# Optimization experiments

Hardware: AMD Instinct MI355X
Metric: run time of the kernel (lower is better)

Reference implementation:

```python
import jax, jax.numpy as jnp
import numpy as np

B, C, N = 2, 1024, 80
D = 3 * C + 2  # 3074 token dim
DFF = 2048     # torch TransformerEncoderLayer default dim_feedforward
HW = 224
REFINE = 3
EPS = 1e-5


def _layernorm(x, g, b):
    m = jnp.mean(x, axis=-1, keepdims=True)
    v = jnp.mean((x - m) ** 2, axis=-1, keepdims=True)
    return g * (x - m) / jnp.sqrt(v + EPS) + b


def _pos_encoding(seq_len, dim):
    pos = jnp.arange(seq_len, dtype=jnp.float32)[:, None]
    div = jnp.exp(jnp.arange(0, dim, 2, dtype=jnp.float32) * (-np.log(10000.0) / dim))
    pe = jnp.zeros((seq_len, dim), dtype=jnp.float32)
    pe = pe.at[:, 0::2].set(jnp.sin(pos * div)).at[:, 1::2].set(jnp.cos(pos * div))
    return pe


def _forward(pre_f, curr_f, first_f, ln_g, ln_b, ipw, ipb, opw, opb,
             n1g, n1b, l1w, l1b, l2w, l2b, n2g, n2b, ow, ob,
             prev_b, first_b):
    # --- vectorized find_best_shift: batched circular L1 correlation ---
    idx = (jnp.arange(N)[None, :] - jnp.arange(N)[:, None]) % N  # [shift, pos]
    rolled = first_b[:, idx]                                     # [B, N, N, 2]
    dist = jnp.abs(prev_b[:, None] - rolled).sum(axis=(-1, -2))  # [B, N]
    best = jnp.argmin(dist, axis=1)                              # first min, like torch loop
    roll_idx = (jnp.arange(N)[None, :] - best[:, None]) % N      # [B, N]
    first_b = jax.vmap(lambda fb, ri: fb[ri])(first_b, roll_idx)

    # --- bilinear upsample to 224x224 (F.interpolate, align_corners=False) ---
    up = lambda f: jax.image.resize(f, (f.shape[0], f.shape[1], HW, HW), method='bilinear')
    pre_up, curr_up, first_up = up(pre_f), up(curr_f), up(first_f)

    # --- vectorized get_bou_features: [B,N,C] gather ---
    gather = jax.vmap(lambda f, b: f[:, b[:, 0], b[:, 1]].T)
    pre_q = gather(pre_up, prev_b)      # [B, N, C]
    first_q = gather(first_up, first_b)  # [B, N, C]

    pe = _pos_encoding(N, D)
    curr = prev_b.astype(jnp.float32)
    scale = 1.0 / jnp.sqrt(jnp.float32(D))
    results = []
    for _ in range(REFINE):
        bf = gather(curr_up, curr.astype(jnp.int32))          # [B, N, C]
        tokens = jnp.concatenate([pre_q, bf, curr, first_q], axis=-1)  # [B, N, D]
        tokens = _layernorm(tokens, ln_g, ln_b)
        tokens = tokens + pe[None]
        # --- TransformerEncoderLayer (post-norm, nhead=1, relu, eval/no dropout) ---
        qkv = tokens @ ipw.T + ipb
        q, k, v = jnp.split(qkv, 3, axis=-1)
        attn = jax.nn.softmax(jnp.einsum('bqd,bkd->bqk', q, k) * scale, axis=-1)
        a = jnp.einsum('bqk,bkd->bqd', attn, v) @ opw.T + opb
        x = _layernorm(tokens + a, n1g, n1b)
        ff = jax.nn.relu(x @ l1w.T + l1b) @ l2w.T + l2b
        x = _layernorm(x + ff, n2g, n2b)
        out = x @ ow.T + ob                                   # [B, N, 1026]
        curr = jnp.clip(curr + out[..., C:], 0.0, 223.0)
        pre_q = pre_q + out[..., :C]
        results.append(curr)
    return jnp.stack(results)  # [REFINE, B, N, 2]


def setup_inputs() -> dict:
    key = jax.random.key(0)
    ks = jax.random.split(key, 12)
    f = lambda i, s: jax.random.normal(ks[i], s, dtype=jnp.float32)
    w = lambda i, s: 0.02 * jax.random.normal(ks[i], s, dtype=jnp.float32)
    return {
        'pre_img_features': f(0, (B, C, 14, 14)),
        'curr_img_features': f(1, (B, C, 14, 14)),
        'first_img_features': f(2, (B, C, 14, 14)),
        'previous_boundary': jax.random.randint(ks[3], (B, N, 2), 0, HW),
        'first_boundary': jax.random.randint(ks[4], (B, N, 2), 0, HW),
        'ln_g': jnp.ones((D,), jnp.float32), 'ln_b': jnp.zeros((D,), jnp.float32),
        'in_proj_w': w(5, (3 * D, D)), 'in_proj_b': jnp.zeros((3 * D,), jnp.float32),
        'out_proj_w': w(6, (D, D)), 'out_proj_b': jnp.zeros((D,), jnp.float32),
        'norm1_g': jnp.ones((D,), jnp.float32), 'norm1_b': jnp.zeros((D,), jnp.float32),
        'lin1_w': w(7, (DFF, D)), 'lin1_b': jnp.zeros((DFF,), jnp.float32),
        'lin2_w': w(8, (D, DFF)), 'lin2_b': jnp.zeros((D,), jnp.float32),
        'norm2_g': jnp.ones((D,), jnp.float32), 'norm2_b': jnp.zeros((D,), jnp.float32),
        'out_w': w(9, (C + 2, D)), 'out_b': jnp.zeros((C + 2,), jnp.float32),
    }


def reference(pre_img_features, curr_img_features, first_img_features,
              previous_boundary, first_boundary,
              ln_g, ln_b, in_proj_w, in_proj_b, out_proj_w, out_proj_b,
              norm1_g, norm1_b, lin1_w, lin1_b, lin2_w, lin2_b,
              norm2_g, norm2_b, out_w, out_b):
    return _forward(pre_img_features, curr_img_features, first_img_features,
                    ln_g, ln_b, in_proj_w, in_proj_b, out_proj_w, out_proj_b,
                    norm1_g, norm1_b, lin1_w, lin1_b, lin2_w, lin2_b,
                    norm2_g, norm2_b, out_w, out_b,
                    previous_boundary, first_boundary)
```

## Files before the change

### kernel.cpp

```cpp
#include <hip/hip_runtime.h>
#include <math.h>

#define B_    2
#define C_    1024
#define N_    80
#define D_    3074
#define DFF_  2048
#define OD_   1026
#define QKV_  9222
#define M_    160
#define EPS_  1e-5f
#define KPD_  3104

typedef __attribute__((ext_vector_type(8))) short bf16x8;
typedef __attribute__((ext_vector_type(4))) float f32x4;

__device__ inline short f2bf(float f) {
    unsigned u = __float_as_uint(f);
    u += 0x7fffu + ((u >> 16) & 1u);
    return (short)(u >> 16);
}

__device__ inline float wave_sum(float v) {
#pragma unroll
    for (int off = 32; off > 0; off >>= 1) v += __shfl_down(v, off, 64);
    return v;
}

__device__ inline float wave_max(float v) {
#pragma unroll
    for (int off = 32; off > 0; off >>= 1) v = fmaxf(v, __shfl_down(v, off, 64));
    return v;
}

__device__ inline void block_reduce_2(float& s, float& s2, float* red) {
    int tid = threadIdx.x;
    int lane = tid & 63, wid = tid >> 6;
    s = wave_sum(s);
    s2 = wave_sum(s2);
    if (lane == 0) { red[wid] = s; red[4 + wid] = s2; }
    __syncthreads();
    if (tid == 0) {
        red[8] = red[0] + red[1] + red[2] + red[3];
        red[9] = red[4] + red[5] + red[6] + red[7];
    }
    __syncthreads();
    s = red[8]; s2 = red[9];
}

__device__ inline void bilin_setup(int p, int& i0, int& i1, float& t) {
    float s = (p + 0.5f) * 0.0625f - 0.5f;
    s = fminf(fmaxf(s, 0.0f), 13.0f);
    i0 = (int)s;
    t = s - (float)i0;
    i1 = min(i0 + 1, 13);
}

__device__ inline float bilin_tap(const float* f, int y0, int y1, float ty,
                                  int x0, int x1, float tx) {
    float a = f[y0 * 14 + x0], b = f[y0 * 14 + x1];
    float c = f[y1 * 14 + x0], d = f[y1 * 14 + x1];
    return (1.f - ty) * ((1.f - tx) * a + tx * b) + ty * ((1.f - tx) * c + tx * d);
}

__global__ __launch_bounds__(128) void align_kernel(const int* __restrict__ prev_b,
                                                    const int* __restrict__ first_b,
                                                    int* __restrict__ fb_al) {
    int b = blockIdx.x;
    int tid = threadIdx.x;
    __shared__ int dist[N_];
    __shared__ int bestIdx;
    if (tid < N_) {
        int s = 0;
        for (int j = 0; j < N_; ++j) {
            int src = (j - tid) % N_;
            if (src < 0) src += N_;
            int dy = prev_b[(b * N_ + j) * 2] - first_b[(b * N_ + src) * 2];
            int dx = prev_b[(b * N_ + j) * 2 + 1] - first_b[(b * N_ + src) * 2 + 1];
            s += abs(dy) + abs(dx);
        }
        dist[tid] = s;
    }
    __syncthreads();
    if (tid == 0) {
        int best = 0, bd = dist[0];
        for (int i = 1; i < N_; ++i)
            if (dist[i] < bd) { bd = dist[i]; best = i; }
        bestIdx = best;
    }
    __syncthreads();
    if (tid < N_) {
        int src = (tid - bestIdx) % N_;
        if (src < 0) src += N_;
        fb_al[(b * N_ + tid) * 2]     = first_b[(b * N_ + src) * 2];
        fb_al[(b * N_ + tid) * 2 + 1] = first_b[(b * N_ + src) * 2 + 1];
    }
}

__global__ __launch_bounds__(256) void gather_init_kernel(
        const float* __restrict__ pre_f, const float* __restrict__ first_f,
        const int* __restrict__ prev_b, const int* __restrict__ fb_al,
        float* __restrict__ pre_q, float* __restrict__ first_q,
        float* __restrict__ curr) {
    int m = blockIdx.x;
    int b = m / N_;
    int tid = threadIdx.x;
    int py = prev_b[m * 2], px = prev_b[m * 2 + 1];
    int fy = fb_al[m * 2], fx = fb_al[m * 2 + 1];
    int py0, py1, px0, px1, fy0, fy1, fx0, fx1;
    float pty, ptx, fty, ftx;
    bilin_setup(py, py0, py1, pty);
    bilin_setup(px, px0, px1, ptx);
    bilin_setup(fy, fy0, fy1, fty);
    bilin_setup(fx, fx0, fx1, ftx);
    for (int c = tid; c < C_; c += 256) {
        const float* fp = pre_f + (size_t)(b * C_ + c) * 196;
        const float* ff = first_f + (size_t)(b * C_ + c) * 196;
        pre_q[(size_t)m * C_ + c]   = bilin_tap(fp, py0, py1, pty, px0, px1, ptx);
        first_q[(size_t)m * C_ + c] = bilin_tap(ff, fy0, fy1, fty, fx0, fx1, ftx);
    }
    if (tid < 2) curr[m * 2 + tid] = (float)prev_b[m * 2 + tid];
}

__global__ __launch_bounds__(256) void tokens_kernel(
        const float* __restrict__ curr_f, const float* __restrict__ pre_q,
        const float* __restrict__ first_q, const float* __restrict__ curr,
        const float* __restrict__ ln_g, const float* __restrict__ ln_b,
        float* __restrict__ tokens, short* __restrict__ tokens_bf) {
    int m = blockIdx.x;
    int b = m / N_;
    int n = m % N_;
    int tid = threadIdx.x;
    __shared__ float bf[C_];
    __shared__ float red[10];

    float cy = curr[m * 2], cx = curr[m * 2 + 1];
    int iy = (int)cy, ix = (int)cx;
    int y0, y1, x0, x1;
    float ty, tx;
    bilin_setup(iy, y0, y1, ty);
    bilin_setup(ix, x0, x1, tx);
    for (int c = tid; c < C_; c += 256) {
        const float* f = curr_f + (size_t)(b * C_ + c) * 196;
        bf[c] = bilin_tap(f, y0, y1, ty, x0, x1, tx);
    }
    __syncthreads();

    float s = 0.f, s2 = 0.f;
    for (int d = tid; d < D_; d += 256) {
        float v;
        if (d < C_)            v = pre_q[(size_t)m * C_ + d];
        else if (d < 2 * C_)   v = bf[d - C_];
        else if (d == 2 * C_)  v = cy;
        else if (d == 2*C_+1)  v = cx;
        else                   v = first_q[(size_t)m * C_ + (d - 2 * C_ - 2)];
        s += v; s2 += v * v;
    }
    block_reduce_2(s, s2, red);
    float mean = s / (float)D_;
    float var = s2 / (float)D_ - mean * mean;
    float inv = rsqrtf(var + EPS_);

    const float negLogDivD = -logf(10000.0f) / (float)D_;
    for (int d = tid; d < KPD_; d += 256) {
        if (d < D_) {
            float v;
            if (d < C_)            v = pre_q[(size_t)m * C_ + d];
            else if (d < 2 * C_)   v = bf[d - C_];
            else if (d == 2 * C_)  v = cy;
            else if (d == 2*C_+1)  v = cx;
            else                   v = first_q[(size_t)m * C_ + (d - 2 * C_ - 2)];
            float ln = ln_g[d] * (v - mean) * inv + ln_b[d];
            int kk = d >> 1;
            float ang = (float)n * expf((float)(2 * kk) * negLogDivD);
            float pe = (d & 1) ? cosf(ang) : sinf(ang);
            float val = ln + pe;
            tokens[(size_t)m * D_ + d] = val;
            tokens_bf[(size_t)m * KPD_ + d] = f2bf(val);
        } else {
            tokens_bf[(size_t)m * KPD_ + d] = 0;
        }
    }
}

__global__ __launch_bounds__(256) void gemm_mfma_sk(
        const short* __restrict__ A, const float* __restrict__ Wf,
        const float* __restrict__ bias, float* __restrict__ Cout,
        int K, int KpA, int O, int KC) {
    int kc0 = blockIdx.y * KC;
    if (kc0 >= K) return;
    int kend = min(K, kc0 + KC);

    int lane = threadIdx.x & 63;
    int wave = threadIdx.x >> 6;
    int col  = lane & 15;
    int quad = lane >> 4;
    int o0 = blockIdx.x * 128 + wave * 32 + col;
    int o1 = o0 + 16;
    int oc0 = min(o0, O - 1), oc1 = min(o1, O - 1);

    const float* wrow0 = Wf + (size_t)oc0 * K + quad * 8;
    const float* wrow1 = Wf + (size_t)oc1 * K + quad * 8;
    const short* abase = A + (size_t)col * KpA + quad * 8;

    f32x4 acc0[10], acc1[10];
#pragma unroll
    for (int t = 0; t < 10; ++t)
#pragma unroll
        for (int r = 0; r < 4; ++r) { acc0[t][r] = 0.f; acc1[t][r] = 0.f; }

    int nfull = (kend - kc0) >> 5;
    bf16x8 aCur[10];
    float2 wCur[8];
    if (nfull > 0) {
#pragma unroll
        for (int t = 0; t < 10; ++t)
            aCur[t] = *(const bf16x8*)(abase + (size_t)t * 16 * KpA + kc0);
#pragma unroll
        for (int j = 0; j < 4; ++j) {
            wCur[j]     = *(const float2*)(wrow0 + kc0 + 2 * j);
            wCur[4 + j] = *(const float2*)(wrow1 + kc0 + 2 * j);
        }
    }
    for (int i = 0; i < nfull; ++i) {
        bf16x8 aNxt[10];
        float2 wNxt[8];
        if (i + 1 < nfull) {
            int kn = kc0 + (i + 1) * 32;
#pragma unroll
            for (int t = 0; t < 10; ++t)
                aNxt[t] = *(const bf16x8*)(abase + (size_t)t * 16 * KpA + kn);
#pragma unroll
            for (int j = 0; j < 4; ++j) {
                wNxt[j]     = *(const float2*)(wrow0 + kn + 2 * j);
                wNxt[4 + j] = *(const float2*)(wrow1 + kn + 2 * j);
            }
        }
        bf16x8 b0, b1;
#pragma unroll
        for (int j = 0; j < 4; ++j) {
            b0[2*j] = f2bf(wCur[j].x);     b0[2*j+1] = f2bf(wCur[j].y);
            b1[2*j] = f2bf(wCur[4+j].x);   b1[2*j+1] = f2bf(wCur[4+j].y);
        }
#pragma unroll
        for (int t = 0; t < 10; ++t) {
            acc0[t] = __builtin_amdgcn_mfma_f32_16x16x32_bf16(aCur[t], b0, acc0[t], 0, 0, 0);
            acc1[t] = __builtin_amdgcn_mfma_f32_16x16x32_bf16(aCur[t], b1, acc1[t], 0, 0, 0);
        }
#pragma unroll
        for (int t = 0; t < 10; ++t) aCur[t] = aNxt[t];
#pragma unroll
        for (int j = 0; j < 8; ++j) wCur[j] = wNxt[j];
    }
    int kmain = kc0 + nfull * 32;
    if (kmain < kend) {
        bf16x8 b0, b1;
#pragma unroll
        for (int j = 0; j < 8; ++j) {
            int k = kmain + quad * 8 + j;
            b0[j] = (k < kend) ? f2bf(Wf[(size_t)oc0 * K + k]) : (short)0;
            b1[j] = (k < kend) ? f2bf(Wf[(size_t)oc1 * K + k]) : (short)0;
        }
#pragma unroll
        for (int t = 0; t < 10; ++t) {
            bf16x8 af = *(const bf16x8*)(abase + (size_t)t * 16 * KpA + kmain);
            acc0[t] = __builtin_amdgcn_mfma_f32_16x16x32_bf16(af, b0, acc0[t], 0, 0, 0);
            acc1[t] = __builtin_amdgcn_mfma_f32_16x16x32_bf16(af, b1, acc1[t], 0, 0, 0);
        }
    }
    if (o0 < O) {
        float bv = (blockIdx.y == 0) ? bias[o0] : 0.f;
#pragma unroll
        for (int t = 0; t < 10; ++t)
#pragma unroll
            for (int r = 0; r < 4; ++r)
                atomicAdd(&Cout[(size_t)(t * 16 + quad * 4 + r) * O + o0], acc0[t][r] + bv);
    }
    if (o1 < O) {
        float bv = (blockIdx.y == 0) ? bias[o1] : 0.f;
#pragma unroll
        for (int t = 0; t < 10; ++t)
#pragma unroll
            for (int r = 0; r < 4; ++r)
                atomicAdd(&Cout[(size_t)(t * 16 + quad * 4 + r) * O + o1], acc1[t][r] + bv);
    }
}

__global__ __launch_bounds__(256) void relu_cvt_kernel(const float* __restrict__ in,
                                                       short* __restrict__ out,
                                                       int n) {
    int i = blockIdx.x * 256 + threadIdx.x;
    if (i < n) out[i] = f2bf(fmaxf(in[i], 0.f));
}

__global__ __launch_bounds__(256) void qkv_cvt_kernel(const float* __restrict__ qkv,
                                                      short* __restrict__ q_bf,
                                                      short* __restrict__ k_bf,
                                                      short* __restrict__ v_bf) {
    int m = blockIdx.x;
    int b = m / N_, q = m % N_;
    const float* src = qkv + (size_t)m * QKV_;
    for (int d = threadIdx.x; d < KPD_; d += 256) {
        short qv = (d < D_) ? f2bf(src[d])          : (short)0;
        short kv = (d < D_) ? f2bf(src[D_ + d])     : (short)0;
        short vv = (d < D_) ? f2bf(src[2 * D_ + d]) : (short)0;
        q_bf[(size_t)m * KPD_ + d] = qv;
        k_bf[(size_t)m * KPD_ + d] = kv;
        v_bf[((size_t)b * 96 + q) * KPD_ + d] = vv;
    }
}

__global__ __launch_bounds__(256) void scores_mfma(const short* __restrict__ q_bf,
                                                   const short* __restrict__ k_bf,
                                                   float* __restrict__ sc) {
    int bi = blockIdx.x;
    int b = bi / 25, qt = (bi % 25) / 5, kt = bi % 5;
    int lane = threadIdx.x & 63, wave = threadIdx.x >> 6;
    int col = lane & 15, quad = lane >> 4;
    const short* qbase = q_bf + (size_t)(b * N_ + qt * 16 + col) * KPD_ + quad * 8;
    const short* kbase = k_bf + (size_t)(b * N_ + kt * 16 + col) * KPD_ + quad * 8;
    f32x4 acc;
#pragma unroll
    for (int r = 0; r < 4; ++r) acc[r] = 0.f;
    int c0 = wave * 25, c1 = min(97, c0 + 25);
    for (int c = c0; c < c1; ++c) {
        bf16x8 af = *(const bf16x8*)(qbase + c * 32);
        bf16x8 bf8 = *(const bf16x8*)(kbase + c * 32);
        acc = __builtin_amdgcn_mfma_f32_16x16x32_bf16(af, bf8, acc, 0, 0, 0);
    }
    __shared__ f32x4 red[4][64];
    red[wave][lane] = acc;
    __syncthreads();
    if (threadIdx.x < 64) {
        f32x4 t = red[0][lane];
#pragma unroll
        for (int w = 1; w < 4; ++w)
#pragma unroll
            for (int r = 0; r < 4; ++r) t[r] += red[w][lane][r];
        float scale = rsqrtf((float)D_);
#pragma unroll
        for (int r = 0; r < 4; ++r)
            sc[(size_t)(b * N_ + qt * 16 + quad * 4 + r) * N_ + kt * 16 + col] = t[r] * scale;
    }
}

__global__ __launch_bounds__(256) void softmax_kernel(const float* __restrict__ sc,
                                                      short* __restrict__ p_bf) {
    int m = blockIdx.x * 4 + (threadIdx.x >> 6);
    int lane = threadIdx.x & 63;
    const float* row = sc + (size_t)m * N_;
    float a = row[lane];
    float bv = (lane < 16) ? row[64 + lane] : -1e30f;
    float mx = wave_max(fmaxf(a, bv));
    mx = __shfl(mx, 0, 64);
    float e0 = expf(a - mx);
    float e1 = (lane < 16) ? expf(bv - mx) : 0.f;
    float sum = wave_sum(e0 + e1);
    sum = __shfl(sum, 0, 64);
    float rs = 1.0f / sum;
    p_bf[(size_t)m * 96 + lane] = f2bf(e0 * rs);
    if (lane < 32)
        p_bf[(size_t)m * 96 + 64 + lane] = (lane < 16) ? f2bf(e1 * rs) : (short)0;
}

__global__ __launch_bounds__(256) void av_mfma(const short* __restrict__ p_bf,
                                               const short* __restrict__ v_bf,
                                               short* __restrict__ av_bf) {
    int bi = blockIdx.x;
    int b = bi / 49, g = bi % 49;
    int lane = threadIdx.x & 63, wave = threadIdx.x >> 6;
    int dtile = g * 4 + wave;
    if (dtile >= 194) return;
    int d0 = dtile * 16;
    int col = lane & 15, quad = lane >> 4;
    const short* pbase = p_bf + (size_t)b * N_ * 96 + quad * 8;
    const short* vb = v_bf + (size_t)b * 96 * KPD_ + d0 + col;
    f32x4 acc[5];
#pragma unroll
    for (int t = 0; t < 5; ++t)
#pragma unroll
        for (int r = 0; r < 4; ++r) acc[t][r] = 0.f;
#pragma unroll
    for (int c = 0; c < 3; ++c) {
        bf16x8 bf8;
#pragma unroll
        for (int j = 0; j < 8; ++j)
            bf8[j] = vb[(size_t)(c * 32 + quad * 8 + j) * KPD_];
#pragma unroll
        for (int t = 0; t < 5; ++t) {
            bf16x8 af = *(const bf16x8*)(pbase + (size_t)(t * 16 + col) * 96 + c * 32);
            acc[t] = __builtin_amdgcn_mfma_f32_16x16x32_bf16(af, bf8, acc[t], 0, 0, 0);
        }
    }
#pragma unroll
    for (int t = 0; t < 5; ++t)
#pragma unroll
        for (int r = 0; r < 4; ++r)
            av_bf[(size_t)(b * N_ + t * 16 + quad * 4 + r) * KPD_ + d0 + col] = f2bf(acc[t][r]);
}

template <bool WF32>
__global__ __launch_bounds__(256) void ln_kernel(const float* __restrict__ xin,
                                                 const float* __restrict__ res,
                                                 const float* __restrict__ g,
                                                 const float* __restrict__ bta,
                                                 float* __restrict__ outf,
                                                 short* __restrict__ outb) {
    int m = blockIdx.x;
    int tid = threadIdx.x;
    __shared__ float red[10];
    const float* xr = xin + (size_t)m * D_;
    const float* rr = res + (size_t)m * D_;
    float s = 0.f, s2 = 0.f;
    for (int d = tid; d < D_; d += 256) {
        float v = xr[d] + rr[d];
        s += v; s2 += v * v;
    }
    block_reduce_2(s, s2, red);
    float mean = s / (float)D_;
    float var = s2 / (float)D_ - mean * mean;
    float inv = rsqrtf(var + EPS_);
    for (int d = tid; d < KPD_; d += 256) {
        if (d < D_) {
            float v = xr[d] + rr[d];
            float y = g[d] * (v - mean) * inv + bta[d];
            if (WF32) outf[(size_t)m * D_ + d] = y;
            outb[(size_t)m * KPD_ + d] = f2bf(y);
        } else {
            outb[(size_t)m * KPD_ + d] = 0;
        }
    }
}

__global__ __launch_bounds__(256) void update_kernel(const float* __restrict__ outb,
                                                     float* __restrict__ curr,
                                                     float* __restrict__ pre_q,
                                                     float* __restrict__ results) {
    int m = blockIdx.x;
    int tid = threadIdx.x;
    for (int c = tid; c < C_; c += 256)
        pre_q[(size_t)m * C_ + c] += outb[(size_t)m * OD_ + c];
    if (tid < 2) {
        float nc = curr[m * 2 + tid] + outb[(size_t)m * OD_ + C_ + tid];
        nc = fminf(fmaxf(nc, 0.f), 223.f);
        curr[m * 2 + tid] = nc;
        results[m * 2 + tid] = nc;
    }
}

extern "C" void kernel_launch(void* const* d_in, const int* in_sizes, int n_in,
                              void* d_out, int out_size, void* d_ws, size_t ws_size,
                              hipStream_t stream) {
    const float* pre_f   = (const float*)d_in[0];
    const float* curr_f  = (const float*)d_in[1];
    const float* first_f = (const float*)d_in[2];
    const int*   prev_b  = (const int*)d_in[3];
    const int*   first_b = (const int*)d_in[4];
    const float* ln_g    = (const float*)d_in[5];
    const float* ln_b    = (const float*)d_in[6];
    const float* ipw     = (const float*)d_in[7];
    const float* ipb     = (const float*)d_in[8];
    const float* opw     = (const float*)d_in[9];
    const float* opb     = (const float*)d_in[10];
    const float* n1g     = (const float*)d_in[11];
    const float* n1b     = (const float*)d_in[12];
    const float* l1w     = (const float*)d_in[13];
    const float* l1b     = (const float*)d_in[14];
    const float* l2w     = (const float*)d_in[15];
    const float* l2b     = (const float*)d_in[16];
    const float* n2g     = (const float*)d_in[17];
    const float* n2b     = (const float*)d_in[18];
    const float* ow      = (const float*)d_in[19];
    const float* ob      = (const float*)d_in[20];
    float* outp = (float*)d_out;

    float* wf = (float*)d_ws;
    size_t off = 0;
    int*   fb_al   = (int*)(wf + off); off += 320;
    float* curr    = wf + off;         off += 320;
    float* pre_q   = wf + off;         off += (size_t)M_ * C_;
    float* first_q = wf + off;         off += (size_t)M_ * C_;
    float* tokens  = wf + off;         off += (size_t)M_ * D_;
    float* qkv     = wf + off;         off += (size_t)M_ * QKV_;
    float* aout    = wf + off;         off += (size_t)M_ * D_;
    float* xbuf    = wf + off;         off += (size_t)M_ * D_;
    float* ff1f    = wf + off;         off += (size_t)M_ * DFF_;
    float* ffout   = wf + off;         off += (size_t)M_ * D_;
    float* outb    = wf + off;         off += (size_t)M_ * OD_;
    float* sc      = wf + off;         off += (size_t)M_ * N_;
    short* tokens_bf = (short*)(wf + off); off += (size_t)M_ * KPD_ / 2;
    short* x_bf      = (short*)(wf + off); off += (size_t)M_ * KPD_ / 2;
    short* x2_bf     = (short*)(wf + off); off += (size_t)M_ * KPD_ / 2;
    short* av_bf     = (short*)(wf + off); off += (size_t)M_ * KPD_ / 2;
    short* ff1_bf    = (short*)(wf + off); off += (size_t)M_ * DFF_ / 2;
    short* q_bf      = (short*)(wf + off); off += (size_t)M_ * KPD_ / 2;
    short* k_bf      = (short*)(wf + off); off += (size_t)M_ * KPD_ / 2;
    short* v_bf      = (short*)(wf + off); off += (size_t)B_ * 96 * KPD_ / 2;
    short* p_bf      = (short*)(wf + off); off += (size_t)M_ * 96 / 2;
    (void)ws_size; (void)in_sizes; (void)n_in; (void)out_size;

    hipLaunchKernelGGL(align_kernel, dim3(B_), dim3(128), 0, stream,
                       prev_b, first_b, fb_al);
    hipLaunchKernelGGL(gather_init_kernel, dim3(M_), dim3(256), 0, stream,
                       pre_f, first_f, prev_b, fb_al, pre_q, first_q, curr);
    hipMemsetAsync(v_bf, 0, (size_t)B_ * 96 * KPD_ * 2, stream);

    for (int it = 0; it < 3; ++it) {
        hipMemsetAsync(qkv,   0, (size_t)M_ * QKV_ * 4, stream);
        hipMemsetAsync(aout,  0, (size_t)M_ * D_   * 4, stream);
        hipMemsetAsync(ff1f,  0, (size_t)M_ * DFF_ * 4, stream);
        hipMemsetAsync(ffout, 0, (size_t)M_ * D_   * 4, stream);
        hipMemsetAsync(outb,  0, (size_t)M_ * OD_  * 4, stream);

        hipLaunchKernelGGL(tokens_kernel, dim3(M_), dim3(256), 0, stream,
                           curr_f, pre_q, first_q, curr, ln_g, ln_b, tokens, tokens_bf);
        hipLaunchKernelGGL(gemm_mfma_sk, dim3(73, 6), dim3(256), 0, stream,
                           tokens_bf, ipw, ipb, qkv, D_, KPD_, QKV_, 544);
        hipLaunchKernelGGL(qkv_cvt_kernel, dim3(M_), dim3(256), 0, stream,
                           qkv, q_bf, k_bf, v_bf);
        hipLaunchKernelGGL(scores_mfma, dim3(50), dim3(256), 0, stream,
                           q_bf, k_bf, sc);
        hipLaunchKernelGGL(softmax_kernel, dim3(40), dim3(256), 0, stream,
                           sc, p_bf);
        hipLaunchKernelGGL(av_mfma, dim3(98), dim3(256), 0, stream,
                           p_bf, v_bf, av_bf);
        hipLaunchKernelGGL(gemm_mfma_sk, dim3(25, 10), dim3(256), 0, stream,
                           av_bf, opw, opb, aout, D_, KPD_, D_, 320);
        hipLaunchKernelGGL((ln_kernel<true>), dim3(M_), dim3(256), 0, stream,
                           tokens, aout, n1g, n1b, xbuf, x_bf);
        hipLaunchKernelGGL(gemm_mfma_sk, dim3(16, 17), dim3(256), 0, stream,
                           x_bf, l1w, l1b, ff1f, D_, KPD_, DFF_, 192);
        hipLaunchKernelGGL(relu_cvt_kernel, dim3((M_ * DFF_ + 255) / 256), dim3(256), 0, stream,
                           ff1f, ff1_bf, M_ * DFF_);
        hipLaunchKernelGGL(gemm_mfma_sk, dim3(25, 11), dim3(256), 0, stream,
                           ff1_bf, l2w, l2b, ffout, DFF_, DFF_, D_, 192);
        hipLaunchKernelGGL((ln_kernel<false>), dim3(M_), dim3(256), 0, stream,
                           xbuf, ffout, n2g, n2b, (float*)nullptr, x2_bf);
        hipLaunchKernelGGL(gemm_mfma_sk, dim3(9, 13), dim3(256), 0, stream,
                           x2_bf, ow, ob, outb, D_, KPD_, OD_, 256);
        hipLaunchKernelGGL(update_kernel, dim3(M_), dim3(256), 0, stream,
                           outb, curr, pre_q, outp + (size_t)it * M_ * 2);
    }
}
```

Measured before the change: 1.159 ms.

## Pre-convert GEMM weights to padded bf16 once and use bf16-weight GEMM

Adds a one-time weight conversion kernel that turns each fp32 weight matrix into a zero-padded bf16 copy in workspace. A new split-K MFMA GEMM reads these bf16 weights directly with a 3-deep register prefetch, so the three refinement iterations fetch half the weight bytes and skip per-use conversion. It also stores V transposed so the AV kernel can do vector loads instead of strided scalar gathers, merges five memsets into one by making the zeroed buffers contiguous, and retunes the split-K grids. The cost is a larger workspace, a fallback path chosen by workspace size, and the up-front conversion pass, which only pays off if it is amortised over the iterations.

Result: slower. 1.367 ms (+17.9%).

```diff
diff --git a/kernel.cpp b/kernel.cpp
--- a/kernel.cpp
+++ b/kernel.cpp
@@ -183,6 +183,84 @@
     }
 }
 
+__global__ __launch_bounds__(256) void wcvt_kernel(const float* __restrict__ W,
+                                                   short* __restrict__ Wb,
+                                                   int K, int KPW) {
+    int o = blockIdx.x;
+    const float* src = W + (size_t)o * K;
+    short* dst = Wb + (size_t)o * KPW;
+    for (int k = threadIdx.x; k < KPW; k += 256)
+        dst[k] = (k < K) ? f2bf(src[k]) : (short)0;
+}
+
+__global__ __launch_bounds__(256) void gemm_bf16_sk(
+        const short* __restrict__ A, const short* __restrict__ Wb,
+        const float* __restrict__ bias, float* __restrict__ Cout,
+        int KPW, int KpA, int O, int KC) {
+    int kc0 = blockIdx.y * KC;
+    if (kc0 >= KPW) return;
+    int nch = (min(KPW, kc0 + KC) - kc0) >> 5;
+
+    int lane = threadIdx.x & 63;
+    int wave = threadIdx.x >> 6;
+    int col  = lane & 15;
+    int quad = lane >> 4;
+    int o0 = blockIdx.x * 128 + wave * 32 + col;
+    int o1 = o0 + 16;
+    int oc0 = min(o0, O - 1), oc1 = min(o1, O - 1);
+    const short* w0 = Wb + (size_t)oc0 * KPW + quad * 8 + kc0;
+    const short* w1 = Wb + (size_t)oc1 * KPW + quad * 8 + kc0;
+    const short* ab = A + (size_t)col * KpA + quad * 8 + kc0;
+
+    f32x4 acc0[10], acc1[10];
+#pragma unroll
+    for (int t = 0; t < 10; ++t)
+#pragma unroll
+        for (int r = 0; r < 4; ++r) { acc0[t][r] = 0.f; acc1[t][r] = 0.f; }
+
+    bf16x8 wb0[3], wb1[3];
+#pragma unroll
+    for (int d = 0; d < 3; ++d)
+        if (d < nch) {
+            wb0[d] = *(const bf16x8*)(w0 + d * 32);
+            wb1[d] = *(const bf16x8*)(w1 + d * 32);
+        }
+    for (int i = 0; i < nch; ++i) {
+        bf16x8 b0 = wb0[0], b1 = wb1[0];
+        wb0[0] = wb0[1]; wb0[1] = wb0[2];
+        wb1[0] = wb1[1]; wb1[1] = wb1[2];
+        if (i + 3 < nch) {
+            wb0[2] = *(const bf16x8*)(w0 + (i + 3) * 32);
+            wb1[2] = *(const bf16x8*)(w1 + (i + 3) * 32);
+        }
+        bf16x8 a[10];
+#pragma unroll
+        for (int t = 0; t < 10; ++t)
+            a[t] = *(const bf16x8*)(ab + (size_t)t * 16 * KpA + i * 32);
+#pragma unroll
+        for (int t = 0; t < 10; ++t) {
+            acc0[t] = __builtin_amdgcn_mfma_f32_16x16x32_bf16(a[t], b0, acc0[t], 0, 0, 0);
+            acc1[t] = __builtin_amdgcn_mfma_f32_16x16x32_bf16(a[t], b1, acc1[t], 0, 0, 0);
+        }
+    }
+    if (o0 < O) {
+        float bv = (blockIdx.y == 0) ? bias[o0] : 0.f;
+#pragma unroll
+        for (int t = 0; t < 10; ++t)
+#pragma unroll
+            for (int r = 0; r < 4; ++r)
+                atomicAdd(&Cout[(size_t)(t * 16 + quad * 4 + r) * O + o0], acc0[t][r] + bv);
+    }
+    if (o1 < O) {
+        float bv = (blockIdx.y == 0) ? bias[o1] : 0.f;
+#pragma unroll
+        for (int t = 0; t < 10; ++t)
+#pragma unroll
+            for (int r = 0; r < 4; ++r)
+                atomicAdd(&Cout[(size_t)(t * 16 + quad * 4 + r) * O + o1], acc1[t][r] + bv);
+    }
+}
+
 __global__ __launch_bounds__(256) void gemm_mfma_sk(
         const short* __restrict__ A, const float* __restrict__ Wf,
         const float* __restrict__ bias, float* __restrict__ Cout,
@@ -296,7 +374,7 @@
 __global__ __launch_bounds__(256) void qkv_cvt_kernel(const float* __restrict__ qkv,
                                                       short* __restrict__ q_bf,
                                                       short* __restrict__ k_bf,
-                                                      short* __restrict__ v_bf) {
+                                                      short* __restrict__ vT) {
     int m = blockIdx.x;
     int b = m / N_, q = m % N_;
     const float* src = qkv + (size_t)m * QKV_;
@@ -306,7 +384,7 @@
         short vv = (d < D_) ? f2bf(src[2 * D_ + d]) : (short)0;
         q_bf[(size_t)m * KPD_ + d] = qv;
         k_bf[(size_t)m * KPD_ + d] = kv;
-        v_bf[((size_t)b * 96 + q) * KPD_ + d] = vv;
+        vT[((size_t)b * KPD_ + d) * 96 + q] = vv;
     }
 }
 
@@ -364,7 +442,7 @@
 }
 
 __global__ __launch_bounds__(256) void av_mfma(const short* __restrict__ p_bf,
-                                               const short* __restrict__ v_bf,
+                                               const short* __restrict__ vT,
                                                short* __restrict__ av_bf) {
     int bi = blockIdx.x;
     int b = bi / 49, g = bi % 49;
@@ -374,7 +452,7 @@
     int d0 = dtile * 16;
     int col = lane & 15, quad = lane >> 4;
     const short* pbase = p_bf + (size_t)b * N_ * 96 + quad * 8;
-    const short* vb = v_bf + (size_t)b * 96 * KPD_ + d0 + col;
+    const short* vb = vT + ((size_t)b * KPD_ + d0 + col) * 96 + quad * 8;
     f32x4 acc[5];
 #pragma unroll
     for (int t = 0; t < 5; ++t)
@@ -382,10 +460,7 @@
         for (int r = 0; r < 4; ++r) acc[t][r] = 0.f;
 #pragma unroll
     for (int c = 0; c < 3; ++c) {
-        bf16x8 bf8;
-#pragma unroll
-        for (int j = 0; j < 8; ++j)
-            bf8[j] = vb[(size_t)(c * 32 + quad * 8 + j) * KPD_];
+        bf16x8 bf8 = *(const bf16x8*)(vb + c * 32);
 #pragma unroll
         for (int t = 0; t < 5; ++t) {
             bf16x8 af = *(const bf16x8*)(pbase + (size_t)(t * 16 + col) * 96 + c * 32);
@@ -483,10 +558,11 @@
     float* tokens  = wf + off;         off += (size_t)M_ * D_;
     float* qkv     = wf + off;         off += (size_t)M_ * QKV_;
     float* aout    = wf + off;         off += (size_t)M_ * D_;
-    float* xbuf    = wf + off;         off += (size_t)M_ * D_;
     float* ff1f    = wf + off;         off += (size_t)M_ * DFF_;
     float* ffout   = wf + off;         off += (size_t)M_ * D_;
     float* outb    = wf + off;         off += (size_t)M_ * OD_;
+    const size_t ZR_BYTES = (size_t)M_ * (QKV_ + D_ + DFF_ + D_ + OD_) * 4;
+    float* xbuf    = wf + off;         off += (size_t)M_ * D_;
     float* sc      = wf + off;         off += (size_t)M_ * N_;
     short* tokens_bf = (short*)(wf + off); off += (size_t)M_ * KPD_ / 2;
     short* x_bf      = (short*)(wf + off); off += (size_t)M_ * KPD_ / 2;
@@ -495,49 +571,83 @@
     short* ff1_bf    = (short*)(wf + off); off += (size_t)M_ * DFF_ / 2;
     short* q_bf      = (short*)(wf + off); off += (size_t)M_ * KPD_ / 2;
     short* k_bf      = (short*)(wf + off); off += (size_t)M_ * KPD_ / 2;
-    short* v_bf      = (short*)(wf + off); off += (size_t)B_ * 96 * KPD_ / 2;
+    short* vT        = (short*)(wf + off); off += (size_t)B_ * KPD_ * 96 / 2;
     short* p_bf      = (short*)(wf + off); off += (size_t)M_ * 96 / 2;
-    (void)ws_size; (void)in_sizes; (void)n_in; (void)out_size;
+    short* ipw_b = (short*)(wf + off); off += (size_t)QKV_ * KPD_ / 2;
+    short* opw_b = (short*)(wf + off); off += (size_t)D_ * KPD_ / 2;
+    short* l1w_b = (short*)(wf + off); off += (size_t)DFF_ * KPD_ / 2;
+    short* l2w_b = (short*)(wf + off); off += (size_t)D_ * DFF_ / 2;
+    short* ow_b  = (short*)(wf + off); off += (size_t)OD_ * KPD_ / 2;
+    const bool useBf16W = ws_size >= off * 4 + 1024;
+    (void)in_sizes; (void)n_in; (void)out_size;
 
     hipLaunchKernelGGL(align_kernel, dim3(B_), dim3(128), 0, stream,
                        prev_b, first_b, fb_al);
     hipLaunchKernelGGL(gather_init_kernel, dim3(M_), dim3(256), 0, stream,
                        pre_f, first_f, prev_b, fb_al, pre_q, first_q, curr);
-    hipMemsetAsync(v_bf, 0, (size_t)B_ * 96 * KPD_ * 2, stream);
+    hipMemsetAsync(vT, 0, (size_t)B_ * KPD_ * 96 * 2, stream);
+    if (useBf16W) {
+        hipLaunchKernelGGL(wcvt_kernel, dim3(QKV_), dim3(256), 0, stream, ipw, ipw_b, D_, KPD_);
+        hipLaunchKernelGGL(wcvt_kernel, dim3(D_),   dim3(256), 0, stream, opw, opw_b, D_, KPD_);
+        hipLaunchKernelGGL(wcvt_kernel, dim3(DFF_), dim3(256), 0, stream, l1w, l1w_b, D_, KPD_);
+        hipLaunchKernelGGL(wcvt_kernel, dim3(D_),   dim3(256), 0, stream, l2w, l2w_b, DFF_, DFF_);
+        hipLaunchKernelGGL(wcvt_kernel, dim3(OD_),  dim3(256), 0, stream, ow,  ow_b,  D_, KPD_);
+    }
 
     for (int it = 0; it < 3; ++it) {
-        hipMemsetAsync(qkv,   0, (size_t)M_ * QKV_ * 4, stream);
-        hipMemsetAsync(aout,  0, (size_t)M_ * D_   * 4, stream);
-        hipMemsetAsync(ff1f,  0, (size_t)M_ * DFF_ * 4, stream);
-        hipMemsetAsync(ffout, 0, (size_t)M_ * D_   * 4, stream);
-        hipMemsetAsync(outb,  0, (size_t)M_ * OD_  * 4, stream);
+        hipMemsetAsync(qkv, 0, ZR_BYTES, stream);
 
         hipLaunchKernelGGL(tokens_kernel, dim3(M_), dim3(256), 0, stream,
                            curr_f, pre_q, first_q, curr, ln_g, ln_b, tokens, tokens_bf);
-        hipLaunchKernelGGL(gemm_mfma_sk, dim3(73, 6), dim3(256), 0, stream,
-                           tokens_bf, ipw, ipb, qkv, D_, KPD_, QKV_, 544);
+        if (useBf16W) {
+            hipLaunchKernelGGL(gemm_bf16_sk, dim3(73, 13), dim3(256), 0, stream,
+                               tokens_bf, ipw_b, ipb, qkv, KPD_, KPD_, QKV_, 256);
+        } else {
+            hipLaunchKernelGGL(gemm_mfma_sk, dim3(73, 13), dim3(256), 0, stream,
+                               tokens_bf, ipw, ipb, qkv, D_, KPD_, QKV_, 256);
+        }
         hipLaunchKernelGGL(qkv_cvt_kernel, dim3(M_), dim3(256), 0, stream,
-                           qkv, q_bf, k_bf, v_bf);
+                           qkv, q_bf, k_bf, vT);
         hipLaunchKernelGGL(scores_mfma, dim3(50), dim3(256), 0, stream,
                            q_bf, k_bf, sc);
         hipLaunchKernelGGL(softmax_kernel, dim3(40), dim3(256), 0, stream,
                            sc, p_bf);
         hipLaunchKernelGGL(av_mfma, dim3(98), dim3(256), 0, stream,
-                           p_bf, v_bf, av_bf);
-        hipLaunchKernelGGL(gemm_mfma_sk, dim3(25, 10), dim3(256), 0, stream,
-                           av_bf, opw, opb, aout, D_, KPD_, D_, 320);
+                           p_bf, vT, av_bf);
+        if (useBf16W) {
+            hipLaunchKernelGGL(gemm_bf16_sk, dim3(25, 13), dim3(256), 0, stream,
+                               av_bf, opw_b, opb, aout, KPD_, KPD_, D_, 256);
+        } else {
+            hipLaunchKernelGGL(gemm_mfma_sk, dim3(25, 13), dim3(256), 0, stream,
+                               av_bf, opw, opb, aout, D_, KPD_, D_, 256);
+        }
         hipLaunchKernelGGL((ln_kernel<true>), dim3(M_), dim3(256), 0, stream,
                            tokens, aout, n1g, n1b, xbuf, x_bf);
-        hipLaunchKernelGGL(gemm_mfma_sk, dim3(16, 17), dim3(256), 0, stream,
-                           x_bf, l1w, l1b, ff1f, D_, KPD_, DFF_, 192);
+        if (useBf16W) {
+            hipLaunchKernelGGL(gemm_bf16_sk, dim3(16, 13), dim3(256), 0, stream,
+                               x_bf, l1w_b, l1b, ff1f, KPD_, KPD_, DFF_, 256);
+        } else {
+            hipLaunchKernelGGL(gemm_mfma_sk, dim3(16, 13), dim3(256), 0, stream,
+                               x_bf, l1w, l1b, ff1f, D_, KPD_, DFF_, 256);
+        }
         hipLaunchKernelGGL(relu_cvt_kernel, dim3((M_ * DFF_ + 255) / 256), dim3(256), 0, stream,
                            ff1f, ff1_bf, M_ * DFF_);
-        hipLaunchKernelGGL(gemm_mfma_sk, dim3(25, 11), dim3(256), 0, stream,
-                           ff1_bf, l2w, l2b, ffout, DFF_, DFF_, D_, 192);
+        if (useBf16W) {
+            hipLaunchKernelGGL(gemm_bf16_sk, dim3(25, 8), dim3(256), 0, stream,
+                               ff1_bf, l2w_b, l2b, ffout, DFF_, DFF_, D_, 256);
+        } else {
+            hipLaunchKernelGGL(gemm_mfma_sk, dim3(25, 8), dim3(256), 0, stream,
+                               ff1_bf, l2w, l2b, ffout, DFF_, DFF_, D_, 256);
+        }
         hipLaunchKernelGGL((ln_kernel<false>), dim3(M_), dim3(256), 0, stream,
                            xbuf, ffout, n2g, n2b, (float*)nullptr, x2_bf);
-        hipLaunchKernelGGL(gemm_mfma_sk, dim3(9, 13), dim3(256), 0, stream,
-                           x2_bf, ow, ob, outb, D_, KPD_, OD_, 256);
+        if (useBf16W) {
+            hipLaunchKernelGGL(gemm_bf16_sk, dim3(9, 13), dim3(256), 0, stream,
+                               x2_bf, ow_b, ob, outb, KPD_, KPD_, OD_, 256);
+        } else {
+            hipLaunchKernelGGL(gemm_mfma_sk, dim3(9, 13), dim3(256), 0, stream,
+                               x2_bf, ow, ob, outb, D_, KPD_, OD_, 256);
+        }
         hipLaunchKernelGGL(update_kernel, dim3(M_), dim3(256), 0, stream,
                            outb, curr, pre_q, outp + (size_t)it * M_ * 2);
     }
```
